# Kernel optimization log

Measured on AMD Instinct MI355X. Metric: run time of the kernel, lower is better.

The kernel has to match this reference:

```python
import jax, jax.numpy as jnp
import numpy as np
from jax import lax

B = 2048


def setup_inputs() -> dict:
    key = jax.random.key(0)
    ks = jax.random.split(key, 12)
    r = lambda k, s, sc=0.05: jax.random.normal(k, s, jnp.float32) * sc
    return {
        "w": jax.random.normal(ks[0], (B, 512), jnp.float32),
        "init_const": r(ks[1], (1, 512, 4, 4), 0.1),
        "init_conv_w": r(ks[2], (256, 512, 3, 3)),
        "init_conv_b": r(ks[3], (256,)),
        "aff1_w": r(ks[4], (256, 512)),
        "aff1_b": r(ks[5], (256,)),
        "conv1_w": r(ks[6], (128, 256, 3, 3)),
        "conv1_b": r(ks[7], (128,)),
        "aff2_w": r(ks[8], (128, 512)),
        "aff2_b": r(ks[9], (128,)),
        "conv2_w": r(ks[10], (64, 128, 3, 3)),
        "conv2_b": r(ks[11], (64,)),
    }


def _conv3(x, W):
    # 3x3 conv, stride 1, padding 1, NCHW / OIHW
    return lax.conv_general_dilated(x, W, (1, 1), ((1, 1), (1, 1)),
                                    dimension_numbers=("NCHW", "OIHW", "NCHW"))


def _lrelu(x):
    return jnp.where(x >= 0, x, 0.2 * x)


def reference(w, init_const, init_conv_w, init_conv_b,
              aff1_w, aff1_b, conv1_w, conv1_b,
              aff2_w, aff2_b, conv2_w, conv2_b):
    batch = w.shape[0]
    x = _conv3(init_const, init_conv_w) + init_conv_b[None, :, None, None]
    x = _lrelu(x)                                   # [1,256,4,4]
    x = jnp.broadcast_to(x, (batch,) + x.shape[1:])  # repeat over batch
    layers = ((aff1_w, aff1_b, conv1_w, conv1_b),
              (aff2_w, aff2_b, conv2_w, conv2_b))
    for aw, ab, cw, cb in layers:
        b_, c, h, wd = x.shape
        # bilinear upsample x2 (half-pixel centers == torch align_corners=False)
        x = jax.image.resize(x, (b_, c, 2 * h, 2 * wd), "bilinear")
        style = w @ aw.T + ab                        # [B, Cin]
        # modulated conv: conv(s*x, W) * demod, where
        # demod[b,o] = rsqrt(sum_{c,k} (s[b,c] W[o,c,k])^2 + 1e-8)
        xm = x * style[:, :, None, None]
        y = _conv3(xm, cw)                           # [B, Cout, 2h, 2w]
        w2 = jnp.sum(cw * cw, axis=(2, 3))           # [Cout, Cin]
        demod = lax.rsqrt(jnp.einsum("bc,oc->bo", style * style, w2) + 1e-8)
        x = _lrelu(y * demod[:, :, None, None] + cb[None, :, None, None])
    return x
```

## Files before the change

### kernel.cpp

```cpp
#include <hip/hip_runtime.h>
#include <hip/hip_fp16.h>

typedef _Float16 f16x8 __attribute__((ext_vector_type(8)));
typedef float f32x4 __attribute__((ext_vector_type(4)));

#define WS_X0U   0
#define WS_GHP   65536
#define WS_W2P   4259840
#define WS_WH    4407296
#define WS_AFTH  6504448
#define WS_W2TH  6897664
#define WS_S1P   7045120
#define WS_S2H   8093696
#define WS_SSQ   8617984
#define WS_D1    10190848
#define WS_D2    11239424
#define WS_X1T   11763712

__device__ __forceinline__ void up_wi(int j, int S, int& i0, int& i1,
                                      float& w0, float& w1) {
  int m = j >> 1;
  if (j & 1) { i0 = m; i1 = (m + 1 < S) ? m + 1 : S - 1; w0 = 0.75f; w1 = 0.25f; }
  else       { i0 = (m - 1 >= 0) ? m - 1 : 0; i1 = m;     w0 = 0.25f; w1 = 0.75f; }
}

__device__ __forceinline__ int xq_off(int pix, int i) {
  return (pix >> 1) * 64 + (((((pix & 1) << 2) + i) ^ ((pix >> 1) & 7)) << 3);
}

__global__ __launch_bounds__(256) void k_init(const float* __restrict__ ic,
    const float* __restrict__ w0c, const float* __restrict__ b0,
    float* __restrict__ x0u) {
  int o = blockIdx.x, t = threadIdx.x;
  int pix = t & 15, cg = t >> 4;
  int py = pix >> 2, px = pix & 3;
  __shared__ float part[16][17];
  __shared__ float x4[16];
  float acc = 0.f;
  int c0 = cg * 32;
  for (int c = c0; c < c0 + 32; ++c) {
    const float* wp = w0c + (o * 512 + c) * 9;
    const float* xp = ic + c * 16;
#pragma unroll
    for (int dy = 0; dy < 3; ++dy) {
      int iy = py + dy - 1;
      if ((unsigned)iy >= 4u) continue;
#pragma unroll
      for (int dx = 0; dx < 3; ++dx) {
        int ix = px + dx - 1;
        if ((unsigned)ix >= 4u) continue;
        acc += wp[dy * 3 + dx] * xp[iy * 4 + ix];
      }
    }
  }
  part[cg][pix] = acc;
  __syncthreads();
  if (t < 16) {
    float v = b0[o];
#pragma unroll
    for (int g = 0; g < 16; ++g) v += part[g][t];
    x4[t] = (v >= 0.f) ? v : 0.2f * v;
  }
  __syncthreads();
  if (t < 64) {
    int oy = t >> 3, ox = t & 7;
    int y0, y1, xx0, xx1; float wy0, wy1, wx0, wx1;
    up_wi(oy, 4, y0, y1, wy0, wy1);
    up_wi(ox, 4, xx0, xx1, wx0, wx1);
    float v = wy0 * (wx0 * x4[y0 * 4 + xx0] + wx1 * x4[y0 * 4 + xx1])
            + wy1 * (wx0 * x4[y1 * 4 + xx0] + wx1 * x4[y1 * 4 + xx1]);
    x0u[o * 64 + t] = v;
  }
}

__global__ __launch_bounds__(256) void k_prep(const float* __restrict__ w1c,
    const float* __restrict__ x0u, _Float16* __restrict__ Ghp) {
  int o = blockIdx.x, pg = blockIdx.y, t = threadIdx.x;
  __shared__ _Float16 x0l[256][66];
  for (int i = t; i < 256 * 64; i += 256) {
    int c = i >> 6, p = i & 63;
    x0l[c][p] = (_Float16)x0u[i];
  }
  __syncthreads();
  int c = t;
  float wr9[9];
#pragma unroll
  for (int k = 0; k < 9; ++k) wr9[k] = w1c[(o * 256 + c) * 9 + k];
  int cpart = ((((c >> 3) & 3) * 16 + (o & 15)) * 8) + (c & 7);
  int cq = c >> 5, oq = o >> 4;
  for (int p = pg * 16; p < pg * 16 + 16; ++p) {
    int py = p >> 3, px = p & 7;
    float acc = 0.f;
#pragma unroll
    for (int dy = 0; dy < 3; ++dy) {
      int iy = py + dy - 1;
      if ((unsigned)iy >= 8u) continue;
#pragma unroll
      for (int dx = 0; dx < 3; ++dx) {
        int ix = px + dx - 1;
        if ((unsigned)ix >= 8u) continue;
        acc += wr9[dy * 3 + dx] * (float)x0l[c][iy * 8 + ix];
      }
    }
    Ghp[((p * 8 + oq) * 8 + cq) * 512 + cpart] = (_Float16)acc;
  }
}

__global__ __launch_bounds__(256) void k_misc(const float* __restrict__ w1c,
    const float* __restrict__ w2c, const float* __restrict__ a1w,
    const float* __restrict__ a2w, const float* __restrict__ wsrc,
    _Float16* __restrict__ w2p, _Float16* __restrict__ wh,
    _Float16* __restrict__ afTh, _Float16* __restrict__ W2Th) {
  int idx = blockIdx.x * 256 + threadIdx.x;
  if (idx < 73728) {
    int tap = idx / 8192, r = idx & 8191;
    int kg = r >> 11, mf = (r >> 9) & 3, l = (r >> 3) & 63, j = r & 7;
    int o = mf * 16 + (l & 15);
    int c = kg * 32 + (l >> 4) * 8 + j;
    w2p[idx] = (_Float16)w2c[(o * 128 + c) * 9 + tap];
  } else if (idx < 73728 + 1048576) {
    int i = idx - 73728;
    wh[i] = (_Float16)wsrc[i];
  } else if (idx < 73728 + 1048576 + 196608) {
    int i = idx - 73728 - 1048576;
    afTh[i] = (_Float16)((i < 131072) ? a1w[i] : a2w[i - 131072]);
  } else if (idx < 73728 + 1048576 + 196608 + 73728) {
    int i = idx - 73728 - 1048576 - 196608;
    int o = i / 384, k = i - o * 384;
    float v = 0.f;
    const float* wp = nullptr;
    if (o < 128 && k < 256)        wp = w1c + (o * 256 + k) * 9;
    else if (o >= 128 && k >= 256) wp = w2c + ((o - 128) * 128 + (k - 256)) * 9;
    if (wp) {
#pragma unroll
      for (int q = 0; q < 9; ++q) v += wp[q] * wp[q];
    }
    W2Th[i] = (_Float16)v;
  }
}

__global__ __launch_bounds__(256) void k_sty(const _Float16* __restrict__ wh,
    const _Float16* __restrict__ afTh, const float* __restrict__ a1b,
    const float* __restrict__ a2b, _Float16* __restrict__ s1p,
    _Float16* __restrict__ s2h, _Float16* __restrict__ ssq) {
  int t = threadIdx.x, lane = t & 63, w = t >> 6;
  int wr = w >> 1, wc = w & 1;
  int b0 = blockIdx.y * 64 + wr * 32;
  int f0 = blockIdx.x * 64 + wc * 32;
  f32x4 acc[2][2] = {};
  int lr = lane & 15, lk = (lane >> 4) * 8;
#pragma unroll
  for (int kg = 0; kg < 16; ++kg) {
    f16x8 af[2], bf[2];
#pragma unroll
    for (int mf = 0; mf < 2; ++mf)
      af[mf] = *(const f16x8*)(wh + (b0 + mf * 16 + lr) * 512 + kg * 32 + lk);
#pragma unroll
    for (int nf = 0; nf < 2; ++nf)
      bf[nf] = *(const f16x8*)(afTh + (f0 + nf * 16 + lr) * 512 + kg * 32 + lk);
#pragma unroll
    for (int mf = 0; mf < 2; ++mf)
#pragma unroll
      for (int nf = 0; nf < 2; ++nf)
        acc[mf][nf] = __builtin_amdgcn_mfma_f32_16x16x32_f16(af[mf], bf[nf], acc[mf][nf], 0, 0, 0);
  }
  int r4 = lane >> 4;
#pragma unroll
  for (int nf = 0; nf < 2; ++nf) {
    int f = f0 + nf * 16 + lr;
    float bias = (f < 256) ? a1b[f] : a2b[f - 256];
#pragma unroll
    for (int mf = 0; mf < 2; ++mf) {
#pragma unroll
      for (int r = 0; r < 4; ++r) {
        int b = b0 + mf * 16 + r4 * 4 + r;
        float v = acc[mf][nf][r] + bias;
        ssq[b * 384 + f] = (_Float16)(v * v);
        if (f < 256) {
          int flat = (((b >> 4) * 8 + (f >> 5)) * 64 + ((f >> 3) & 3) * 16 + (b & 15)) * 8 + (f & 7);
          s1p[flat] = (_Float16)v;
        } else {
          s2h[b * 128 + (f - 256)] = (_Float16)v;
        }
      }
    }
  }
}

__global__ __launch_bounds__(256) void k_dmd(const _Float16* __restrict__ ssq,
    const _Float16* __restrict__ W2Th, float* __restrict__ d1,
    float* __restrict__ d2) {
  int t = threadIdx.x, lane = t & 63, w = t >> 6;
  int wr = w >> 1, wc = w & 1;
  int b0 = blockIdx.y * 64 + wr * 32;
  int o0 = blockIdx.x * 64 + wc * 32;
  int kbeg = (blockIdx.x == 2) ? 8 : 0;
  int kend = (blockIdx.x == 2) ? 12 : 8;
  f32x4 acc[2][2] = {};
  int lr = lane & 15, lk = (lane >> 4) * 8;
  for (int kg = kbeg; kg < kend; ++kg) {
    f16x8 af[2], bf[2];
#pragma unroll
    for (int mf = 0; mf < 2; ++mf)
      af[mf] = *(const f16x8*)(ssq + (b0 + mf * 16 + lr) * 384 + kg * 32 + lk);
#pragma unroll
    for (int nf = 0; nf < 2; ++nf)
      bf[nf] = *(const f16x8*)(W2Th + (o0 + nf * 16 + lr) * 384 + kg * 32 + lk);
#pragma unroll
    for (int mf = 0; mf < 2; ++mf)
#pragma unroll
      for (int nf = 0; nf < 2; ++nf)
        acc[mf][nf] = __builtin_amdgcn_mfma_f32_16x16x32_f16(af[mf], bf[nf], acc[mf][nf], 0, 0, 0);
  }
  int r4 = lane >> 4;
#pragma unroll
  for (int mf = 0; mf < 2; ++mf) {
#pragma unroll
    for (int r = 0; r < 4; ++r) {
      int b = b0 + mf * 16 + r4 * 4 + r;
#pragma unroll
      for (int nf = 0; nf < 2; ++nf) {
        int o = o0 + nf * 16 + lr;
        float v = rsqrtf(acc[mf][nf][r] + 1e-8f);
        if (o < 128) d1[b * 128 + o] = v;
        else         d2[b * 64 + (o - 128)] = v;
      }
    }
  }
}

__global__ __launch_bounds__(256) void k_l1(const _Float16* __restrict__ s1p,
    const _Float16* __restrict__ Ghp, const float* __restrict__ d1,
    const float* __restrict__ c1b, const _Float16* __restrict__ s2h,
    __half* __restrict__ x1t) {
  int t = threadIdx.x, lane = t & 63, w = t >> 6;
  int wr = w >> 1, wc = w & 1;
  int bq0 = blockIdx.y * 8 + wr * 4;
  int nq0 = blockIdx.x * 8 + wc * 4;
  f32x4 acc[4][4] = {};
#pragma unroll
  for (int kg = 0; kg < 8; ++kg) {
    f16x8 af[4], bf[4];
#pragma unroll
    for (int mf = 0; mf < 4; ++mf)
      af[mf] = *(const f16x8*)(s1p + (((bq0 + mf) * 8 + kg) * 64 + lane) * 8);
#pragma unroll
    for (int nf = 0; nf < 4; ++nf)
      bf[nf] = *(const f16x8*)(Ghp + (((nq0 + nf) * 8 + kg) * 64 + lane) * 8);
#pragma unroll
    for (int mf = 0; mf < 4; ++mf)
#pragma unroll
      for (int nf = 0; nf < 4; ++nf)
        acc[mf][nf] = __builtin_amdgcn_mfma_f32_16x16x32_f16(af[mf], bf[nf], acc[mf][nf], 0, 0, 0);
  }
  int nc = lane & 15, r4 = lane >> 4;
#pragma unroll
  for (int mf = 0; mf < 4; ++mf) {
#pragma unroll
    for (int r = 0; r < 4; ++r) {
      int b = (bq0 + mf) * 16 + r4 * 4 + r;
#pragma unroll
      for (int nf = 0; nf < 4; ++nf) {
        int n = (nq0 + nf) * 16 + nc;
        int o = n & 127, p = n >> 7;
        float v = acc[mf][nf][r] * d1[b * 128 + o] + c1b[o];
        v = (v >= 0.f) ? v : 0.2f * v;
        v *= (float)s2h[b * 128 + o];
        x1t[(b * 64 + p) * 128 + o] = (__half)v;
      }
    }
  }
}

__global__ __launch_bounds__(256, 2) void k_l2(const __half* __restrict__ x1t,
    const float* __restrict__ d2g, const _Float16* __restrict__ w2p,
    const float* __restrict__ c2b, float* __restrict__ out) {
  int b = blockIdx.x, t = threadIdx.x;
  int lane = t & 63, w = t >> 6;
  __shared__ unsigned short xq[2][9792];
  __shared__ unsigned short x1l[64 * 128];
  const __half* xb = x1t + b * 8192;

  for (int idx = t; idx < 1024; idx += 256) {
    int q = idx >> 4, gc = idx & 15;
    f16x8 v = *(const f16x8*)(xb + q * 128 + gc * 8);
    int gs = (gc & 8) | ((gc ^ q) & 7);
    *(f16x8*)&x1l[q * 128 + gs * 8] = v;
  }
  {
    f16x8 z = {};
    for (int idx = t; idx < 400; idx += 256) {
      int pg = idx >> 3, g = idx & 7;
      int buf = g >> 2, i = g & 3;
      int pix;
      if (pg < 18) pix = 288 + pg;
      else { int j = pg - 18; pix = (j >> 1) * 18 + (j & 1) * 17; }
      *(f16x8*)&xq[buf][xq_off(pix, i)] = z;
    }
  }
  f16x8 afb[3][4];
#pragma unroll
  for (int mf = 0; mf < 4; ++mf) {
    afb[0][mf] = *(const f16x8*)(w2p + (((0 * 4 + 0) * 4 + mf) * 64 + lane) * 8);
    afb[1][mf] = *(const f16x8*)(w2p + (((1 * 4 + 0) * 4 + mf) * 64 + lane) * 8);
  }
  int fy = t >> 4, fx = t & 15;
  int y0, y1, x0, x1i; float wy0, wy1, wx0, wx1;
  up_wi(fy, 8, y0, y1, wy0, wy1);
  up_wi(fx, 8, x0, x1i, wx0, wx1);
  _Float16 wA = (_Float16)(wy0 * wx0), wB = (_Float16)(wy0 * wx1);
  _Float16 wC = (_Float16)(wy1 * wx0), wD = (_Float16)(wy1 * wx1);
  int pixb = fy * 18 + fx + 1;
  int q00 = y0 * 8 + x0, q01 = y0 * 8 + x1i, q10 = y1 * 8 + x0, q11 = y1 * 8 + x1i;

  auto build_granule = [&](int qn, int i) {
    int gc = qn * 4 + i;
    f16x8 va = *(const f16x8*)&x1l[q00 * 128 + ((gc & 8) | ((gc ^ q00) & 7)) * 8];
    f16x8 vb = *(const f16x8*)&x1l[q01 * 128 + ((gc & 8) | ((gc ^ q01) & 7)) * 8];
    f16x8 vc = *(const f16x8*)&x1l[q10 * 128 + ((gc & 8) | ((gc ^ q10) & 7)) * 8];
    f16x8 vd = *(const f16x8*)&x1l[q11 * 128 + ((gc & 8) | ((gc ^ q11) & 7)) * 8];
    f16x8 v = va * wA;
    v += vb * wB;
    v += vc * wC;
    v += vd * wD;
    *(f16x8*)&xq[qn & 1][xq_off(pixb, i)] = v;
  };

  __syncthreads();
#pragma unroll
  for (int i = 0; i < 4; ++i) build_granule(0, i);
  __syncthreads();

  f32x4 acc[4][4] = {};
  f16x8 bfb[2][4];
  int ig = lane >> 4;

#pragma unroll
  for (int q = 0; q < 4; ++q) {
#pragma unroll
    for (int nf = 0; nf < 4; ++nf) {
      int fr = w * 4 + nf - 1;
      int srow = ((unsigned)fr < 16u) ? fr : 16;
      int pix = srow * 18 + (lane & 15);
      bfb[0][nf] = *(const f16x8*)&xq[q & 1][xq_off(pix, ig)];
    }
#pragma unroll
    for (int s = 0; s < 9; ++s) {
      const int S = q * 9 + s;
      if (s < 8) {
        int tapn = s + 1;
        int dyn = tapn / 3, dxn = tapn - dyn * 3;
#pragma unroll
        for (int nf = 0; nf < 4; ++nf) {
          int fr = w * 4 + nf + dyn - 1;
          int srow = ((unsigned)fr < 16u) ? fr : 16;
          int pix = srow * 18 + (lane & 15) + dxn;
          bfb[(s + 1) & 1][nf] = *(const f16x8*)&xq[q & 1][xq_off(pix, ig)];
        }
      }
      if (S < 34) {
        int Sn = S + 2;
        int qn2 = Sn / 9, tapn = Sn - qn2 * 9;
#pragma unroll
        for (int mf = 0; mf < 4; ++mf)
          afb[Sn % 3][mf] = *(const f16x8*)(w2p + (((tapn * 4 + qn2) * 4 + mf) * 64 + lane) * 8);
      }
      if (q < 3 && (s & 1) && s < 8)
        build_granule(q + 1, (s - 1) >> 1);
      __builtin_amdgcn_s_setprio(1);
#pragma unroll
      for (int mf = 0; mf < 4; ++mf)
#pragma unroll
        for (int nf = 0; nf < 4; ++nf)
          acc[mf][nf] = __builtin_amdgcn_mfma_f32_16x16x32_f16(afb[S % 3][mf], bfb[s & 1][nf], acc[mf][nf], 0, 0, 0);
      __builtin_amdgcn_s_setprio(0);
    }
    if (q < 3) __syncthreads();
  }
  int px = lane & 15, r4 = lane >> 4;
#pragma unroll
  for (int mf = 0; mf < 4; ++mf) {
#pragma unroll
    for (int r = 0; r < 4; ++r) {
      int o = mf * 16 + r4 * 4 + r;
      float dm = d2g[b * 64 + o], bias = c2b[o];
#pragma unroll
      for (int nf = 0; nf < 4; ++nf) {
        int py = w * 4 + nf;
        float v = acc[mf][nf][r] * dm + bias;
        v = (v >= 0.f) ? v : 0.2f * v;
        out[(b * 64 + o) * 256 + py * 16 + px] = v;
      }
    }
  }
}

extern "C" void kernel_launch(void* const* d_in, const int* in_sizes, int n_in,
                              void* d_out, int out_size, void* d_ws, size_t ws_size,
                              hipStream_t stream) {
  const float* w    = (const float*)d_in[0];
  const float* ic   = (const float*)d_in[1];
  const float* w0c  = (const float*)d_in[2];
  const float* b0   = (const float*)d_in[3];
  const float* a1w  = (const float*)d_in[4];
  const float* a1b  = (const float*)d_in[5];
  const float* w1c  = (const float*)d_in[6];
  const float* c1b  = (const float*)d_in[7];
  const float* a2w  = (const float*)d_in[8];
  const float* a2b  = (const float*)d_in[9];
  const float* w2c  = (const float*)d_in[10];
  const float* c2b  = (const float*)d_in[11];
  float* out = (float*)d_out;
  char* ws = (char*)d_ws;

  float*    x0u  = (float*)(ws + WS_X0U);
  _Float16* Ghp  = (_Float16*)(ws + WS_GHP);
  _Float16* w2p  = (_Float16*)(ws + WS_W2P);
  _Float16* wh   = (_Float16*)(ws + WS_WH);
  _Float16* afTh = (_Float16*)(ws + WS_AFTH);
  _Float16* W2Th = (_Float16*)(ws + WS_W2TH);
  _Float16* s1p  = (_Float16*)(ws + WS_S1P);
  _Float16* s2h  = (_Float16*)(ws + WS_S2H);
  _Float16* ssq  = (_Float16*)(ws + WS_SSQ);
  float*    d1   = (float*)(ws + WS_D1);
  float*    d2   = (float*)(ws + WS_D2);
  __half*   x1t  = (__half*)(ws + WS_X1T);

  k_init <<<256, 256, 0, stream>>>(ic, w0c, b0, x0u);
  dim3 gp(128, 4);
  k_prep <<<gp, 256, 0, stream>>>(w1c, x0u, Ghp);
  k_misc <<<5440, 256, 0, stream>>>(w1c, w2c, a1w, a2w, w, w2p, wh, afTh, W2Th);
  dim3 gs(6, 32);
  k_sty  <<<gs, 256, 0, stream>>>(wh, afTh, a1b, a2b, s1p, s2h, ssq);
  dim3 gd(3, 32);
  k_dmd  <<<gd, 256, 0, stream>>>(ssq, W2Th, d1, d2);
  dim3 g1(64, 16);
  k_l1   <<<g1, 256, 0, stream>>>(s1p, Ghp, d1, c1b, s2h, x1t);
  k_l2   <<<2048, 256, 0, stream>>>(x1t, d2, w2p, c2b, out);
}
```

Before: 156.0 us.

## Reuse 6-row LDS window across dy taps in second modulated conv

Reorders the 3x3 tap loop to iterate dx outer and dy inner. For each dx the kernel loads a 6-row window of B fragments once and reuses it for all three dy taps, instead of reloading 4 rows per tap. This cuts LDS reads from 36 to 18 fragments per channel quarter. It costs more registers for the window, and the weight prefetch order and granule-build schedule are remapped to match.

```diff
diff --git a/kernel.cpp b/kernel.cpp
--- a/kernel.cpp
+++ b/kernel.cpp
@@ -302,7 +302,7 @@
 #pragma unroll
   for (int mf = 0; mf < 4; ++mf) {
     afb[0][mf] = *(const f16x8*)(w2p + (((0 * 4 + 0) * 4 + mf) * 64 + lane) * 8);
-    afb[1][mf] = *(const f16x8*)(w2p + (((1 * 4 + 0) * 4 + mf) * 64 + lane) * 8);
+    afb[1][mf] = *(const f16x8*)(w2p + (((3 * 4 + 0) * 4 + mf) * 64 + lane) * 8);
   }
   int fy = t >> 4, fx = t & 15;
   int y0, y1, x0, x1i; float wy0, wy1, wx0, wx1;
@@ -332,48 +332,51 @@
   __syncthreads();
 
   f32x4 acc[4][4] = {};
-  f16x8 bfb[2][4];
+  f16x8 rw[2][6];
   int ig = lane >> 4;
+  int colb = lane & 15;
+
+  auto read_win = [&](int qb, int buf, int dx) {
+#pragma unroll
+    for (int j = 0; j < 6; ++j) {
+      int fr = w * 4 + j - 1;
+      int srow = ((unsigned)fr < 16u) ? fr : 16;
+      int pix = srow * 18 + colb + dx;
+      rw[buf][j] = *(const f16x8*)&xq[qb][xq_off(pix, ig)];
+    }
+  };
 
 #pragma unroll
   for (int q = 0; q < 4; ++q) {
-#pragma unroll
-    for (int nf = 0; nf < 4; ++nf) {
-      int fr = w * 4 + nf - 1;
-      int srow = ((unsigned)fr < 16u) ? fr : 16;
-      int pix = srow * 18 + (lane & 15);
-      bfb[0][nf] = *(const f16x8*)&xq[q & 1][xq_off(pix, ig)];
-    }
-#pragma unroll
-    for (int s = 0; s < 9; ++s) {
-      const int S = q * 9 + s;
-      if (s < 8) {
-        int tapn = s + 1;
-        int dyn = tapn / 3, dxn = tapn - dyn * 3;
-#pragma unroll
-        for (int nf = 0; nf < 4; ++nf) {
-          int fr = w * 4 + nf + dyn - 1;
-          int srow = ((unsigned)fr < 16u) ? fr : 16;
-          int pix = srow * 18 + (lane & 15) + dxn;
-          bfb[(s + 1) & 1][nf] = *(const f16x8*)&xq[q & 1][xq_off(pix, ig)];
+    read_win(q & 1, 0, 0);
+#pragma unroll
+    for (int dx = 0; dx < 3; ++dx) {
+      if (dx < 2) read_win(q & 1, (dx + 1) & 1, dx + 1);
+      if (q < 3) {
+        if (dx == 0) { build_granule(q + 1, 0); build_granule(q + 1, 1); }
+        else if (dx == 1) build_granule(q + 1, 2);
+        else              build_granule(q + 1, 3);
+      }
+#pragma unroll
+      for (int dy = 0; dy < 3; ++dy) {
+        const int u = q * 9 + dx * 3 + dy;
+        if (u + 2 < 36) {
+          const int un = u + 2;
+          const int qn = un / 9, rn = un - qn * 9;
+          const int dxn = rn / 3, dyn = rn - dxn * 3;
+          const int tapn = dyn * 3 + dxn;
+#pragma unroll
+          for (int mf = 0; mf < 4; ++mf)
+            afb[un % 3][mf] = *(const f16x8*)(w2p + (((tapn * 4 + qn) * 4 + mf) * 64 + lane) * 8);
         }
-      }
-      if (S < 34) {
-        int Sn = S + 2;
-        int qn2 = Sn / 9, tapn = Sn - qn2 * 9;
+        __builtin_amdgcn_s_setprio(1);
 #pragma unroll
         for (int mf = 0; mf < 4; ++mf)
-          afb[Sn % 3][mf] = *(const f16x8*)(w2p + (((tapn * 4 + qn2) * 4 + mf) * 64 + lane) * 8);
-      }
-      if (q < 3 && (s & 1) && s < 8)
-        build_granule(q + 1, (s - 1) >> 1);
-      __builtin_amdgcn_s_setprio(1);
-#pragma unroll
-      for (int mf = 0; mf < 4; ++mf)
-#pragma unroll
-        for (int nf = 0; nf < 4; ++nf)
-          acc[mf][nf] = __builtin_amdgcn_mfma_f32_16x16x32_f16(afb[S % 3][mf], bfb[s & 1][nf], acc[mf][nf], 0, 0, 0);
-      __builtin_amdgcn_s_setprio(0);
+#pragma unroll
+          for (int nf = 0; nf < 4; ++nf)
+            acc[mf][nf] = __builtin_amdgcn_mfma_f32_16x16x32_f16(afb[u % 3][mf], rw[dx & 1][nf + dy], acc[mf][nf], 0, 0, 0);
+        __builtin_amdgcn_s_setprio(0);
+      }
     }
     if (q < 3) __syncthreads();
   }
```

After: 155.5 us. No clear change (-0.3%).
